# Kernel optimization log

Hardware: AMD Instinct MI355X
Metric: run time of the kernel (lower is better)

## Reference

```python
import jax, jax.numpy as jnp
import numpy as np

D_MODEL = 1024
NUM_HEADS = 16
D_HEAD = D_MODEL // NUM_HEADS
BATCH = 4
SEQ = 2048
NEG_INF = -1e30


def setup_inputs() -> dict:
    key = jax.random.key(0)
    k_x, k_q, k_k, k_v, k_o = jax.random.split(key, 5)
    scale = 1.0 / np.sqrt(D_MODEL)
    x = jax.random.normal(k_x, (BATCH, SEQ, D_MODEL), dtype=jnp.float32)
    Qw = jax.random.normal(k_q, (D_MODEL, D_MODEL), dtype=jnp.float32) * scale
    Kw = jax.random.normal(k_k, (D_MODEL, D_MODEL), dtype=jnp.float32) * scale
    Vw = jax.random.normal(k_v, (D_MODEL, D_MODEL), dtype=jnp.float32) * scale
    Ow = jax.random.normal(k_o, (D_MODEL, D_MODEL), dtype=jnp.float32) * scale
    padding_mask = jnp.zeros((BATCH, SEQ), dtype=bool)  # True = masked position
    return {"x": x, "Qw": Qw, "Kw": Kw, "Vw": Vw, "Ow": Ow, "padding_mask": padding_mask}


def reference(x, Qw, Kw, Vw, Ow, padding_mask):
    B, S, D = x.shape
    H, dh = NUM_HEADS, D_HEAD
    # torch Linear (no bias): y = x @ W.T
    q = jnp.einsum("bsd,ed->bse", x, Qw).reshape(B, S, H, dh)
    k = jnp.einsum("bsd,ed->bse", x, Kw).reshape(B, S, H, dh)
    v = jnp.einsum("bsd,ed->bse", x, Vw).reshape(B, S, H, dh)
    # scores: [B, H, Sq, Sk]
    score = jnp.einsum("bqhd,bkhd->bhqk", q, k) / jnp.sqrt(jnp.float32(dh))
    # causal mask (masked=True)
    causal = jnp.tril(jnp.ones((S, S), dtype=bool))  # True = keep
    score = jnp.where(causal[None, None, :, :], score, NEG_INF)
    # padding mask: True = masked key position
    score = jnp.where(padding_mask[:, None, None, :], NEG_INF, score)
    attn = jax.nn.softmax(score, axis=-1)  # dropout=0.0 (eval mode)
    ctx = jnp.einsum("bhqk,bkhd->bqhd", attn, v).reshape(B, S, D)
    out = jnp.einsum("bsd,ed->bse", ctx, Ow)
    return out
```

## Files before the change

### kernel.cpp

```cpp
#include <hip/hip_runtime.h>
#include <hip/hip_bf16.h>

typedef __attribute__((ext_vector_type(8))) short short8;
typedef __attribute__((ext_vector_type(4))) float f32x4;

#define MFMA_BF16_16x16x32(a,b,c) __builtin_amdgcn_mfma_f32_16x16x32_bf16((a),(b),(c),0,0,0)

constexpr int B_  = 4;
constexpr int S_  = 2048;
constexpr int H_  = 16;
constexpr int DH_ = 64;
constexpr int D_  = 1024;
constexpr int M_  = B_ * S_;

__device__ __forceinline__ unsigned short f2bf(float f) {
  union { float f; unsigned u; } v; v.f = f;
  unsigned u = v.u;
  u += 0x7fffu + ((u >> 16) & 1u);
  return (unsigned short)(u >> 16);
}

__device__ __forceinline__ short8 cvt8(f32x4 a, f32x4 b) {
  union { __hip_bfloat162 h[4]; short8 s; } u;
  u.h[0] = __float22bfloat162_rn(make_float2(a[0], a[1]));
  u.h[1] = __float22bfloat162_rn(make_float2(a[2], a[3]));
  u.h[2] = __float22bfloat162_rn(make_float2(b[0], b[1]));
  u.h[3] = __float22bfloat162_rn(make_float2(b[2], b[3]));
  return u.s;
}

__global__ __launch_bounds__(256)
void gemm_qkv(const float* __restrict__ x,
              const float* __restrict__ Qw, const float* __restrict__ Kw,
              const float* __restrict__ Vw,
              unsigned short* __restrict__ Qo, unsigned short* __restrict__ Ko,
              unsigned short* __restrict__ VTo) {
  constexpr int BM = 128, BK = 32, LDK = 40;
  __shared__ __align__(16) short As[BM * LDK];
  __shared__ __align__(16) short Bs[BM * LDK];

  const int nb = blockIdx.x;
  const float* W;
  unsigned short* out;
  float scale = 1.0f;
  int epi;
  if (nb < 8)       { W = Qw; out = Qo;  scale = 0.125f; epi = 1; }
  else if (nb < 16) { W = Kw; out = Ko;  epi = 1; }
  else              { W = Vw; out = VTo; epi = 2; }

  const int tid  = threadIdx.x;
  const int lane = tid & 63;
  const int w    = tid >> 6;
  const int quad = lane >> 4;
  const int l16  = lane & 15;
  const int wm   = (w >> 1) * 64;
  const int wn   = (w & 1) * 64;

  const int m0 = blockIdx.y * BM;
  const int n0 = (nb & 7) * 128;

  f32x4 acc[4][4];
  #pragma unroll
  for (int i = 0; i < 4; ++i)
    #pragma unroll
    for (int j = 0; j < 4; ++j)
      acc[i][j] = (f32x4){0.f, 0.f, 0.f, 0.f};

  for (int k0 = 0; k0 < D_; k0 += BK) {
    __syncthreads();
    #pragma unroll
    for (int i = 0; i < 2; ++i) {
      int flat = i * 256 + tid;
      int row  = flat >> 2;
      int col  = (flat & 3) * 8;
      const float* Ap = x + (size_t)(m0 + row) * D_ + k0 + col;
      *(short8*)(&As[row * LDK + col]) = cvt8(*(const f32x4*)Ap, *(const f32x4*)(Ap + 4));
      const float* Wp = W + (size_t)(n0 + row) * D_ + k0 + col;
      *(short8*)(&Bs[row * LDK + col]) = cvt8(*(const f32x4*)Wp, *(const f32x4*)(Wp + 4));
    }
    __syncthreads();

    short8 af[4], bf[4];
    #pragma unroll
    for (int i = 0; i < 4; ++i)
      af[i] = *(const short8*)(&As[(wm + i * 16 + l16) * LDK + quad * 8]);
    #pragma unroll
    for (int j = 0; j < 4; ++j)
      bf[j] = *(const short8*)(&Bs[(wn + j * 16 + l16) * LDK + quad * 8]);
    #pragma unroll
    for (int i = 0; i < 4; ++i)
      #pragma unroll
      for (int j = 0; j < 4; ++j)
        acc[i][j] = MFMA_BF16_16x16x32(af[i], bf[j], acc[i][j]);
  }

  #pragma unroll
  for (int i = 0; i < 4; ++i)
    #pragma unroll
    for (int j = 0; j < 4; ++j)
      #pragma unroll
      for (int r = 0; r < 4; ++r) {
        int m = m0 + wm + i * 16 + quad * 4 + r;
        int n = n0 + wn + j * 16 + l16;
        unsigned short bv = f2bf(acc[i][j][r] * scale);
        int b = m >> 11, s = m & (S_ - 1);
        int h = n >> 6,  d = n & (DH_ - 1);
        if (epi == 1)
          out[((size_t)(b * H_ + h) * S_ + s) * DH_ + d] = bv;
        else
          out[((size_t)(b * H_ + h) * DH_ + d) * S_ + s] = bv;
      }
}

__global__ __launch_bounds__(256)
void gemm_out(const unsigned short* __restrict__ A,
              const float* __restrict__ W,
              float* __restrict__ out) {
  constexpr int BM = 128, BK = 32, LDK = 40;
  __shared__ __align__(16) short As[BM * LDK];
  __shared__ __align__(16) short Bs[BM * LDK];

  const int tid  = threadIdx.x;
  const int lane = tid & 63;
  const int w    = tid >> 6;
  const int quad = lane >> 4;
  const int l16  = lane & 15;
  const int wm   = (w >> 1) * 64;
  const int wn   = (w & 1) * 64;

  const int m0 = blockIdx.y * BM;
  const int n0 = blockIdx.x * 128;

  f32x4 acc[4][4];
  #pragma unroll
  for (int i = 0; i < 4; ++i)
    #pragma unroll
    for (int j = 0; j < 4; ++j)
      acc[i][j] = (f32x4){0.f, 0.f, 0.f, 0.f};

  for (int k0 = 0; k0 < D_; k0 += BK) {
    __syncthreads();
    #pragma unroll
    for (int i = 0; i < 2; ++i) {
      int flat = i * 256 + tid;
      int row  = flat >> 2;
      int col  = (flat & 3) * 8;
      *(short8*)(&As[row * LDK + col]) =
          *(const short8*)(A + (size_t)(m0 + row) * D_ + k0 + col);
      const float* Wp = W + (size_t)(n0 + row) * D_ + k0 + col;
      *(short8*)(&Bs[row * LDK + col]) = cvt8(*(const f32x4*)Wp, *(const f32x4*)(Wp + 4));
    }
    __syncthreads();

    short8 af[4], bf[4];
    #pragma unroll
    for (int i = 0; i < 4; ++i)
      af[i] = *(const short8*)(&As[(wm + i * 16 + l16) * LDK + quad * 8]);
    #pragma unroll
    for (int j = 0; j < 4; ++j)
      bf[j] = *(const short8*)(&Bs[(wn + j * 16 + l16) * LDK + quad * 8]);
    #pragma unroll
    for (int i = 0; i < 4; ++i)
      #pragma unroll
      for (int j = 0; j < 4; ++j)
        acc[i][j] = MFMA_BF16_16x16x32(af[i], bf[j], acc[i][j]);
  }

  #pragma unroll
  for (int i = 0; i < 4; ++i)
    #pragma unroll
    for (int j = 0; j < 4; ++j)
      #pragma unroll
      for (int r = 0; r < 4; ++r) {
        int m = m0 + wm + i * 16 + quad * 4 + r;
        int n = n0 + wn + j * 16 + l16;
        out[(size_t)m * D_ + n] = acc[i][j][r];
      }
}

__global__ __launch_bounds__(256)
void attn(const unsigned short* __restrict__ Q,
          const unsigned short* __restrict__ K,
          const unsigned short* __restrict__ VT,
          const unsigned char* __restrict__ pmask,
          unsigned short* __restrict__ CTX) {
  constexpr int LDP = 72;
  __shared__ __align__(16) short Ps[4 * 32 * LDP];

  const int tid  = threadIdx.x;
  const int lane = tid & 63;
  const int w    = tid >> 6;
  const int quad = lane >> 4;
  const int l16  = lane & 15;

  const int L    = blockIdx.x;
  const int xcd  = L & 7;
  const int slot = L >> 3;
  const int bh   = xcd + 8 * (slot & 7);
  const int xp   = slot >> 3;
  const int b    = bh >> 4;
  const int h    = bh & 15;
  const int pair = xp * 4 + w;

  const unsigned short* Qh = Q  + ((size_t)b * H_ + h) * S_ * DH_;
  const unsigned short* Kh = K  + ((size_t)b * H_ + h) * S_ * DH_;
  const unsigned short* Vh = VT + ((size_t)b * H_ + h) * DH_ * S_;
  const unsigned char* pmb = pmask + (size_t)b * S_;
  unsigned short* CTXb = CTX + (size_t)b * S_ * D_;
  short* Pw = &Ps[w * 32 * LDP];

  for (int half = 0; half < 2; ++half) {
    const int qt = half ? (63 - pair) : pair;
    const int qw = qt * 32;

    short8 qf[2][2];
    #pragma unroll
    for (int i = 0; i < 2; ++i)
      #pragma unroll
      for (int c = 0; c < 2; ++c)
        qf[i][c] = *(const short8*)(Qh + (size_t)(qw + i * 16 + l16) * DH_ + c * 32 + quad * 8);

    f32x4 acc[2][4];
    float mrow[2][4], lrow[2][4];
    #pragma unroll
    for (int i = 0; i < 2; ++i)
      #pragma unroll
      for (int t = 0; t < 4; ++t) acc[i][t] = (f32x4){0.f, 0.f, 0.f, 0.f};
    #pragma unroll
    for (int i = 0; i < 2; ++i)
      #pragma unroll
      for (int r = 0; r < 4; ++r) { mrow[i][r] = -1e30f; lrow[i][r] = 0.f; }

    const int ntiles = (qw >> 6) + 1;

    short8 kb[8];
    #pragma unroll
    for (int t = 0; t < 4; ++t) {
      const unsigned short* kp = Kh + (size_t)(t * 16 + l16) * DH_ + quad * 8;
      kb[t * 2]     = *(const short8*)(kp);
      kb[t * 2 + 1] = *(const short8*)(kp + 32);
    }

    for (int kt = 0; kt < ntiles; ++kt) {
      const int k0 = kt * 64;
      const bool last = (kt == ntiles - 1);

      unsigned char pd[4];
      #pragma unroll
      for (int t = 0; t < 4; ++t) pd[t] = pmb[k0 + t * 16 + l16];

      f32x4 sc[2][4];
      __builtin_amdgcn_s_setprio(1);
      #pragma unroll
      for (int t = 0; t < 4; ++t) {
        #pragma unroll
        for (int i = 0; i < 2; ++i) {
          f32x4 z = (f32x4){0.f, 0.f, 0.f, 0.f};
          z = MFMA_BF16_16x16x32(qf[i][0], kb[t * 2], z);
          sc[i][t] = MFMA_BF16_16x16x32(qf[i][1], kb[t * 2 + 1], z);
        }
      }
      __builtin_amdgcn_s_setprio(0);

      short8 vb[8];
      #pragma unroll
      for (int ks = 0; ks < 2; ++ks)
        #pragma unroll
        for (int t = 0; t < 4; ++t)
          vb[ks * 4 + t] = *(const short8*)(Vh + (size_t)(t * 16 + l16) * S_ +
                                            k0 + ks * 32 + quad * 8);
      {
        const int kn0 = (last ? k0 : k0 + 64);
        #pragma unroll
        for (int t = 0; t < 4; ++t) {
          const unsigned short* kp = Kh + (size_t)(kn0 + t * 16 + l16) * DH_ + quad * 8;
          kb[t * 2]     = *(const short8*)(kp);
          kb[t * 2 + 1] = *(const short8*)(kp + 32);
        }
      }

      float pb[4];
      #pragma unroll
      for (int t = 0; t < 4; ++t) pb[t] = pd[t] ? -1e30f : 0.f;
      #pragma unroll
      for (int t = 0; t < 4; ++t)
        #pragma unroll
        for (int i = 0; i < 2; ++i)
          #pragma unroll
          for (int r = 0; r < 4; ++r)
            sc[i][t][r] += pb[t];
      if (last) {
        #pragma unroll
        for (int t = 0; t < 4; ++t) {
          int key = k0 + t * 16 + l16;
          #pragma unroll
          for (int i = 0; i < 2; ++i)
            #pragma unroll
            for (int r = 0; r < 4; ++r) {
              int qrow = qw + i * 16 + quad * 4 + r;
              if (key > qrow) sc[i][t][r] = -1e30f;
            }
        }
      }

      #pragma unroll
      for (int i = 0; i < 2; ++i)
        #pragma unroll
        for (int r = 0; r < 4; ++r) {
          float rm = fmaxf(fmaxf(sc[i][0][r], sc[i][1][r]), fmaxf(sc[i][2][r], sc[i][3][r]));
          #pragma unroll
          for (int off = 8; off; off >>= 1) rm = fmaxf(rm, __shfl_xor(rm, off, 16));
          float mnew = fmaxf(mrow[i][r], rm);
          float al = __expf(mrow[i][r] - mnew);
          float rs = 0.f;
          #pragma unroll
          for (int t = 0; t < 4; ++t) {
            float p = __expf(sc[i][t][r] - mnew);
            sc[i][t][r] = p;
            rs += p;
          }
          #pragma unroll
          for (int off = 8; off; off >>= 1) rs += __shfl_xor(rs, off, 16);
          lrow[i][r] = lrow[i][r] * al + rs;
          mrow[i][r] = mnew;
          #pragma unroll
          for (int t = 0; t < 4; ++t) acc[i][t][r] *= al;
        }

      #pragma unroll
      for (int i = 0; i < 2; ++i)
        #pragma unroll
        for (int t = 0; t < 4; ++t)
          #pragma unroll
          for (int r = 0; r < 4; ++r)
            Pw[(i * 16 + quad * 4 + r) * LDP + t * 16 + l16] = (short)f2bf(sc[i][t][r]);

      __builtin_amdgcn_s_setprio(1);
      #pragma unroll
      for (int ks = 0; ks < 2; ++ks) {
        short8 pa0 = *(const short8*)(&Pw[l16 * LDP + ks * 32 + quad * 8]);
        short8 pa1 = *(const short8*)(&Pw[(16 + l16) * LDP + ks * 32 + quad * 8]);
        #pragma unroll
        for (int t = 0; t < 4; ++t) {
          acc[0][t] = MFMA_BF16_16x16x32(pa0, vb[ks * 4 + t], acc[0][t]);
          acc[1][t] = MFMA_BF16_16x16x32(pa1, vb[ks * 4 + t], acc[1][t]);
        }
      }
      __builtin_amdgcn_s_setprio(0);
    }

    #pragma unroll
    for (int i = 0; i < 2; ++i)
      #pragma unroll
      for (int r = 0; r < 4; ++r) {
        int qrow = qw + i * 16 + quad * 4 + r;
        float inv = 1.0f / lrow[i][r];
        #pragma unroll
        for (int t = 0; t < 4; ++t)
          CTXb[(size_t)qrow * D_ + h * DH_ + t * 16 + l16] = f2bf(acc[i][t][r] * inv);
      }
  }
}

extern "C" void kernel_launch(void* const* d_in, const int* in_sizes, int n_in,
                              void* d_out, int out_size, void* d_ws, size_t ws_size,
                              hipStream_t stream) {
  const float* x  = (const float*)d_in[0];
  const float* Qw = (const float*)d_in[1];
  const float* Kw = (const float*)d_in[2];
  const float* Vw = (const float*)d_in[3];
  const float* Ow = (const float*)d_in[4];
  const unsigned char* pm = (const unsigned char*)d_in[5];

  const size_t NE = (size_t)M_ * D_;
  unsigned short* Qall  = (unsigned short*)d_out;
  unsigned short* CTXa  = (unsigned short*)d_out + NE;
  unsigned short* Kall  = (unsigned short*)d_ws;
  unsigned short* VTall = (unsigned short*)d_ws + NE;

  gemm_qkv<<<dim3(24, M_ / 128), 256, 0, stream>>>(x, Qw, Kw, Vw,
                                                   Qall, Kall, VTall);

  attn<<<dim3(512), 256, 0, stream>>>(Qall, Kall, VTall, pm, CTXa);

  hipMemcpyAsync(d_ws, (const void*)CTXa, NE * sizeof(unsigned short),
                 hipMemcpyDeviceToDevice, stream);

  gemm_out<<<dim3(D_ / 128, M_ / 128), 256, 0, stream>>>((unsigned short*)d_ws,
                                                         Ow, (float*)d_out);
}
```

Before: 424.1 us.

## Shrink attention wave tile to 16 rows, double grid, add lazy rescale and MFMA row sums

Each wave in the attention kernel now handles a 16-row query tile instead of 32, and the grid doubles to 1024 blocks with a launch_bounds occupancy hint of 4. The online softmax only rescales when the row max rises by more than 8, skipping most exp/multiply work, and the row-sum is computed by an MFMA against a ones vector instead of shuffles. The K prefetch for the next tile is removed, so K loads now sit in the critical path. Halving the tile also halves K/V reuse per wave, which raises memory traffic in exchange for better parallelism and lower register pressure.

```diff
diff --git a/kernel.cpp b/kernel.cpp
--- a/kernel.cpp
+++ b/kernel.cpp
@@ -178,14 +178,14 @@
       }
 }
 
-__global__ __launch_bounds__(256)
+__global__ __launch_bounds__(256, 4)
 void attn(const unsigned short* __restrict__ Q,
           const unsigned short* __restrict__ K,
           const unsigned short* __restrict__ VT,
           const unsigned char* __restrict__ pmask,
           unsigned short* __restrict__ CTX) {
   constexpr int LDP = 72;
-  __shared__ __align__(16) short Ps[4 * 32 * LDP];
+  __shared__ __align__(16) short Ps[4 * 16 * LDP];
 
   const int tid  = threadIdx.x;
   const int lane = tid & 63;
@@ -207,58 +207,53 @@
   const unsigned short* Vh = VT + ((size_t)b * H_ + h) * DH_ * S_;
   const unsigned char* pmb = pmask + (size_t)b * S_;
   unsigned short* CTXb = CTX + (size_t)b * S_ * D_;
-  short* Pw = &Ps[w * 32 * LDP];
+  short* Pw = &Ps[w * 16 * LDP];
+
+  const short8 ones = {0x3F80, 0x3F80, 0x3F80, 0x3F80,
+                       0x3F80, 0x3F80, 0x3F80, 0x3F80};
 
   for (int half = 0; half < 2; ++half) {
-    const int qt = half ? (63 - pair) : pair;
-    const int qw = qt * 32;
-
-    short8 qf[2][2];
-    #pragma unroll
-    for (int i = 0; i < 2; ++i)
-      #pragma unroll
-      for (int c = 0; c < 2; ++c)
-        qf[i][c] = *(const short8*)(Qh + (size_t)(qw + i * 16 + l16) * DH_ + c * 32 + quad * 8);
-
-    f32x4 acc[2][4];
-    float mrow[2][4], lrow[2][4];
-    #pragma unroll
-    for (int i = 0; i < 2; ++i)
-      #pragma unroll
-      for (int t = 0; t < 4; ++t) acc[i][t] = (f32x4){0.f, 0.f, 0.f, 0.f};
-    #pragma unroll
-    for (int i = 0; i < 2; ++i)
-      #pragma unroll
-      for (int r = 0; r < 4; ++r) { mrow[i][r] = -1e30f; lrow[i][r] = 0.f; }
+    const int qt = half ? (127 - pair) : pair;
+    const int qw = qt * 16;
+
+    short8 qf[2];
+    #pragma unroll
+    for (int c = 0; c < 2; ++c)
+      qf[c] = *(const short8*)(Qh + (size_t)(qw + l16) * DH_ + c * 32 + quad * 8);
+
+    f32x4 acc[4];
+    f32x4 lacc;
+    float mrow[4];
+    #pragma unroll
+    for (int t = 0; t < 4; ++t) acc[t] = (f32x4){0.f, 0.f, 0.f, 0.f};
+    lacc = (f32x4){0.f, 0.f, 0.f, 0.f};
+    #pragma unroll
+    for (int r = 0; r < 4; ++r) mrow[r] = -1e30f;
 
     const int ntiles = (qw >> 6) + 1;
-
-    short8 kb[8];
-    #pragma unroll
-    for (int t = 0; t < 4; ++t) {
-      const unsigned short* kp = Kh + (size_t)(t * 16 + l16) * DH_ + quad * 8;
-      kb[t * 2]     = *(const short8*)(kp);
-      kb[t * 2 + 1] = *(const short8*)(kp + 32);
-    }
 
     for (int kt = 0; kt < ntiles; ++kt) {
       const int k0 = kt * 64;
       const bool last = (kt == ntiles - 1);
 
+      short8 kb[8];
+      #pragma unroll
+      for (int t = 0; t < 4; ++t) {
+        const unsigned short* kp = Kh + (size_t)(k0 + t * 16 + l16) * DH_ + quad * 8;
+        kb[t * 2]     = *(const short8*)(kp);
+        kb[t * 2 + 1] = *(const short8*)(kp + 32);
+      }
       unsigned char pd[4];
       #pragma unroll
       for (int t = 0; t < 4; ++t) pd[t] = pmb[k0 + t * 16 + l16];
 
-      f32x4 sc[2][4];
+      f32x4 sc[4];
       __builtin_amdgcn_s_setprio(1);
       #pragma unroll
       for (int t = 0; t < 4; ++t) {
-        #pragma unroll
-        for (int i = 0; i < 2; ++i) {
-          f32x4 z = (f32x4){0.f, 0.f, 0.f, 0.f};
-          z = MFMA_BF16_16x16x32(qf[i][0], kb[t * 2], z);
-          sc[i][t] = MFMA_BF16_16x16x32(qf[i][1], kb[t * 2 + 1], z);
-        }
+        f32x4 z = (f32x4){0.f, 0.f, 0.f, 0.f};
+        z = MFMA_BF16_16x16x32(qf[0], kb[t * 2], z);
+        sc[t] = MFMA_BF16_16x16x32(qf[1], kb[t * 2 + 1], z);
       }
       __builtin_amdgcn_s_setprio(0);
 
@@ -269,96 +264,79 @@
         for (int t = 0; t < 4; ++t)
           vb[ks * 4 + t] = *(const short8*)(Vh + (size_t)(t * 16 + l16) * S_ +
                                             k0 + ks * 32 + quad * 8);
-      {
-        const int kn0 = (last ? k0 : k0 + 64);
-        #pragma unroll
-        for (int t = 0; t < 4; ++t) {
-          const unsigned short* kp = Kh + (size_t)(kn0 + t * 16 + l16) * DH_ + quad * 8;
-          kb[t * 2]     = *(const short8*)(kp);
-          kb[t * 2 + 1] = *(const short8*)(kp + 32);
-        }
-      }
-
-      float pb[4];
-      #pragma unroll
-      for (int t = 0; t < 4; ++t) pb[t] = pd[t] ? -1e30f : 0.f;
-      #pragma unroll
-      for (int t = 0; t < 4; ++t)
-        #pragma unroll
-        for (int i = 0; i < 2; ++i)
-          #pragma unroll
-          for (int r = 0; r < 4; ++r)
-            sc[i][t][r] += pb[t];
+
+      #pragma unroll
+      for (int t = 0; t < 4; ++t) {
+        float pb = pd[t] ? -1e30f : 0.f;
+        #pragma unroll
+        for (int r = 0; r < 4; ++r) sc[t][r] += pb;
+      }
       if (last) {
         #pragma unroll
         for (int t = 0; t < 4; ++t) {
           int key = k0 + t * 16 + l16;
           #pragma unroll
-          for (int i = 0; i < 2; ++i)
-            #pragma unroll
-            for (int r = 0; r < 4; ++r) {
-              int qrow = qw + i * 16 + quad * 4 + r;
-              if (key > qrow) sc[i][t][r] = -1e30f;
-            }
+          for (int r = 0; r < 4; ++r) {
+            int qrow = qw + quad * 4 + r;
+            if (key > qrow) sc[t][r] = -1e30f;
+          }
         }
       }
 
-      #pragma unroll
-      for (int i = 0; i < 2; ++i)
+      float rm[4];
+      #pragma unroll
+      for (int r = 0; r < 4; ++r) {
+        float m = fmaxf(fmaxf(sc[0][r], sc[1][r]), fmaxf(sc[2][r], sc[3][r]));
+        #pragma unroll
+        for (int off = 8; off; off >>= 1) m = fmaxf(m, __shfl_xor(m, off, 16));
+        rm[r] = m;
+      }
+      bool grow = false;
+      #pragma unroll
+      for (int r = 0; r < 4; ++r) grow = grow || (rm[r] > mrow[r] + 8.f);
+      if (__all(!grow) == 0) {
         #pragma unroll
         for (int r = 0; r < 4; ++r) {
-          float rm = fmaxf(fmaxf(sc[i][0][r], sc[i][1][r]), fmaxf(sc[i][2][r], sc[i][3][r]));
+          float mnew = fmaxf(mrow[r], rm[r]);
+          float al = __expf(mrow[r] - mnew);
           #pragma unroll
-          for (int off = 8; off; off >>= 1) rm = fmaxf(rm, __shfl_xor(rm, off, 16));
-          float mnew = fmaxf(mrow[i][r], rm);
-          float al = __expf(mrow[i][r] - mnew);
-          float rs = 0.f;
-          #pragma unroll
-          for (int t = 0; t < 4; ++t) {
-            float p = __expf(sc[i][t][r] - mnew);
-            sc[i][t][r] = p;
-            rs += p;
-          }
-          #pragma unroll
-          for (int off = 8; off; off >>= 1) rs += __shfl_xor(rs, off, 16);
-          lrow[i][r] = lrow[i][r] * al + rs;
-          mrow[i][r] = mnew;
-          #pragma unroll
-          for (int t = 0; t < 4; ++t) acc[i][t][r] *= al;
+          for (int t = 0; t < 4; ++t) acc[t][r] *= al;
+          lacc[r] *= al;
+          mrow[r] = mnew;
         }
-
-      #pragma unroll
-      for (int i = 0; i < 2; ++i)
+      }
+      #pragma unroll
+      for (int t = 0; t < 4; ++t)
+        #pragma unroll
+        for (int r = 0; r < 4; ++r)
+          sc[t][r] = __expf(sc[t][r] - mrow[r]);
+
+      #pragma unroll
+      for (int t = 0; t < 4; ++t)
+        #pragma unroll
+        for (int r = 0; r < 4; ++r)
+          Pw[(quad * 4 + r) * LDP + t * 16 + l16] = (short)f2bf(sc[t][r]);
+
+      __builtin_amdgcn_s_setprio(1);
+      #pragma unroll
+      for (int ks = 0; ks < 2; ++ks) {
+        short8 pa = *(const short8*)(&Pw[l16 * LDP + ks * 32 + quad * 8]);
         #pragma unroll
         for (int t = 0; t < 4; ++t)
-          #pragma unroll
-          for (int r = 0; r < 4; ++r)
-            Pw[(i * 16 + quad * 4 + r) * LDP + t * 16 + l16] = (short)f2bf(sc[i][t][r]);
-
-      __builtin_amdgcn_s_setprio(1);
-      #pragma unroll
-      for (int ks = 0; ks < 2; ++ks) {
-        short8 pa0 = *(const short8*)(&Pw[l16 * LDP + ks * 32 + quad * 8]);
-        short8 pa1 = *(const short8*)(&Pw[(16 + l16) * LDP + ks * 32 + quad * 8]);
-        #pragma unroll
-        for (int t = 0; t < 4; ++t) {
-          acc[0][t] = MFMA_BF16_16x16x32(pa0, vb[ks * 4 + t], acc[0][t]);
-          acc[1][t] = MFMA_BF16_16x16x32(pa1, vb[ks * 4 + t], acc[1][t]);
-        }
+          acc[t] = MFMA_BF16_16x16x32(pa, vb[ks * 4 + t], acc[t]);
+        lacc = MFMA_BF16_16x16x32(pa, ones, lacc);
       }
       __builtin_amdgcn_s_setprio(0);
     }
 
     #pragma unroll
-    for (int i = 0; i < 2; ++i)
-      #pragma unroll
-      for (int r = 0; r < 4; ++r) {
-        int qrow = qw + i * 16 + quad * 4 + r;
-        float inv = 1.0f / lrow[i][r];
-        #pragma unroll
-        for (int t = 0; t < 4; ++t)
-          CTXb[(size_t)qrow * D_ + h * DH_ + t * 16 + l16] = f2bf(acc[i][t][r] * inv);
-      }
+    for (int r = 0; r < 4; ++r) {
+      int qrow = qw + quad * 4 + r;
+      float inv = 1.0f / lacc[r];
+      #pragma unroll
+      for (int t = 0; t < 4; ++t)
+        CTXb[(size_t)qrow * D_ + h * DH_ + t * 16 + l16] = f2bf(acc[t][r] * inv);
+    }
   }
 }
 
@@ -381,7 +359,7 @@
   gemm_qkv<<<dim3(24, M_ / 128), 256, 0, stream>>>(x, Qw, Kw, Vw,
                                                    Qall, Kall, VTall);
 
-  attn<<<dim3(512), 256, 0, stream>>>(Qall, Kall, VTall, pm, CTXa);
+  attn<<<dim3(1024), 256, 0, stream>>>(Qall, Kall, VTall, pm, CTXa);
 
   hipMemcpyAsync(d_ws, (const void*)CTXa, NE * sizeof(unsigned short),
                  hipMemcpyDeviceToDevice, stream);
```

Measured after the change: 491.9 us. 1.16x slower.
